# Performance work log

Hardware: AMD Instinct MI355X
Metric: run time of the kernel (lower is better)

## Reference

```python
import jax, jax.numpy as jnp
import numpy as np

C_IN, C_INT = 256, 128


def setup_inputs() -> dict:
    key = jax.random.key(0)
    ks = jax.random.split(key, 7)
    B, H, W = 8, 64, 64
    s_in = 1.0 / np.sqrt(C_IN)
    return {
        "x": jax.random.normal(ks[0], (B, C_IN, H, W), dtype=jnp.float32),
        "w_theta": jax.random.uniform(ks[1], (C_INT, C_IN), jnp.float32, -s_in, s_in),
        "b_theta": jax.random.uniform(ks[2], (C_INT,), jnp.float32, -s_in, s_in),
        "w_phi": jax.random.uniform(ks[3], (C_INT, C_IN), jnp.float32, -s_in, s_in),
        "b_phi": jax.random.uniform(ks[4], (C_INT,), jnp.float32, -s_in, s_in),
        "w_g": jax.random.uniform(ks[5], (C_INT, C_IN), jnp.float32, -s_in, s_in),
        "b_g": jax.random.uniform(ks[6], (C_INT,), jnp.float32, -s_in, s_in),
    }


def reference(x, w_theta, b_theta, w_phi, b_phi, w_g, b_g):
    B, C, H, W = x.shape
    # flatten spatial: [B, N, C], 1x1 conv == per-position linear
    xf = x.reshape(B, C, H * W).transpose(0, 2, 1)  # [B, N, C_in]
    theta = jnp.einsum('bnc,dc->bnd', xf, w_theta) + b_theta  # [B, N, C_int]
    phi = jnp.einsum('bnc,dc->bnd', xf, w_phi) + b_phi        # [B, N, C_int]
    g = jnp.einsum('bnc,dc->bnd', xf, w_g) + b_g              # [B, N, C_int]
    f = jnp.einsum('bnd,bmd->bnm', theta, phi)  # [B, N, N] unscaled scores
    f_div_C = jax.nn.softmax(f, axis=-1)
    y = jnp.einsum('bnm,bmd->bnd', f_div_C, g)  # [B, N, C_int]
    # back to [B, C_int, H, W]
    return y.transpose(0, 2, 1).reshape(B, C_INT, H, W)
```

## Files before the change

kernel.cpp:

```cpp
#include <hip/hip_runtime.h>

typedef __attribute__((ext_vector_type(8))) short bf8;
typedef __attribute__((ext_vector_type(4))) float f4;
typedef unsigned short u16;

constexpr int B_ = 8, CIN = 256, CINT = 128, NN = 4096;
constexpr float L2E = 1.44269504088896f;

__device__ __forceinline__ u16 f2bf(float f) {
  unsigned int u = __builtin_bit_cast(unsigned int, f);
  u += 0x7FFFu + ((u >> 16) & 1u);
  return (u16)(u >> 16);
}

__device__ __forceinline__ void glds16(const void* g, void* l) {
  __builtin_amdgcn_global_load_lds(
      (const __attribute__((address_space(1))) unsigned int*)g,
      (__attribute__((address_space(3))) unsigned int*)l, 16, 0, 0);
}

__device__ __forceinline__ int cvtpk(float lo, float hi) {
  int r;
  asm("v_cvt_pk_bf16_f32 %0, %1, %2" : "=v"(r) : "v"(lo), "v"(hi));
  return r;
}

__global__ __launch_bounds__(256) void prep_kernel(
    const float* __restrict__ wth, const float* __restrict__ wph,
    const float* __restrict__ wg, u16* __restrict__ wbf)
{
  int i = blockIdx.x * 256 + threadIdx.x;
  const float* src = (i < 32768) ? wth : (i < 65536) ? wph : wg;
  wbf[i] = f2bf(src[i & 32767]);
}

__global__ __launch_bounds__(256) void proj_kernel(
    const float* __restrict__ x, const u16* __restrict__ wbf,
    const float* __restrict__ bth, const float* __restrict__ bph,
    const float* __restrict__ bg,
    u16* __restrict__ theta, u16* __restrict__ phiT, u16* __restrict__ gTt)
{
  const int b = blockIdx.y, n0 = blockIdx.x * 64;
  const int tid = threadIdx.x, w = tid >> 6, l = tid & 63;
  const int lr = l & 15, lg = l >> 4;
  __shared__ __align__(16) u16 sx[64 * 256];

  const float* xb = x + (size_t)b * CIN * NN + n0;
  #pragma unroll
  for (int pass = 0; pass < 8; ++pass) {
    const int cb = w * 8 + pass * 32;
    u16 tmp[8];
    #pragma unroll
    for (int i = 0; i < 8; ++i) tmp[i] = f2bf(xb[(size_t)(cb + i) * NN + l]);
    uint4 v;
    v.x = (unsigned)tmp[0] | ((unsigned)tmp[1] << 16);
    v.y = (unsigned)tmp[2] | ((unsigned)tmp[3] << 16);
    v.z = (unsigned)tmp[4] | ((unsigned)tmp[5] << 16);
    v.w = (unsigned)tmp[6] | ((unsigned)tmp[7] << 16);
    *(uint4*)&sx[l * 256 + (((w + pass * 4) ^ (l & 7)) << 3)] = v;
  }
  __syncthreads();

  #pragma unroll
  for (int dti = 0; dti < 6; ++dti) {
    const int dt = w * 6 + dti;
    const int mat = dt >> 3, d0 = (dt & 7) * 16;
    const float* Bv = (mat == 0) ? bth : (mat == 1) ? bph : bg;
    const u16* wrow = wbf + mat * 32768 + (size_t)(d0 + lr) * 256 + lg * 8;
    bf8 wf[8];
    #pragma unroll
    for (int ks = 0; ks < 8; ++ks) wf[ks] = *(const bf8*)(wrow + ks * 32);

    #pragma unroll
    for (int mt = 0; mt < 4; ++mt) {
      f4 acc = {0.f, 0.f, 0.f, 0.f};
      const int row = mt * 16 + lr;
      #pragma unroll
      for (int ks = 0; ks < 8; ++ks) {
        bf8 bx = *(const bf8*)&sx[row * 256 + (((ks * 4 + lg) ^ (lr & 7)) << 3)];
        acc = __builtin_amdgcn_mfma_f32_16x16x32_bf16(wf[ks], bx, acc, 0, 0, 0);
      }
      const int m = n0 + mt * 16 + lr;
      const int dlo = d0 + lg * 4;
      if (mat == 0) {
        ushort4 h4;
        h4.x = f2bf(acc[0] + Bv[dlo + 0]);
        h4.y = f2bf(acc[1] + Bv[dlo + 1]);
        h4.z = f2bf(acc[2] + Bv[dlo + 2]);
        h4.w = f2bf(acc[3] + Bv[dlo + 3]);
        *(ushort4*)&theta[((size_t)b * NN + m) * CINT + dlo] = h4;
      } else if (mat == 1) {
        const int kt = m >> 5, r32 = m & 31;
        ushort4 h4;
        h4.x = f2bf((acc[0] + Bv[dlo + 0]) * L2E);
        h4.y = f2bf((acc[1] + Bv[dlo + 1]) * L2E);
        h4.z = f2bf((acc[2] + Bv[dlo + 2]) * L2E);
        h4.w = f2bf((acc[3] + Bv[dlo + 3]) * L2E);
        *(ushort4*)&phiT[((size_t)(b * 128 + kt)) * 4096 + r32 * 128 +
                         ((((dlo >> 3) ^ (r32 & 7))) << 3) + (dlo & 7)] = h4;
      } else {
        const int kt = m >> 5, kk = m & 31;
        #pragma unroll
        for (int r = 0; r < 4; ++r) {
          const int d = dlo + r;
          const int grow = d >> 1;
          const int chunk = (((d & 1) * 4 + (kk >> 3)) ^ (grow & 7));
          gTt[((size_t)(b * 128 + kt)) * 4096 + grow * 64 + chunk * 8 + (kk & 7)]
              = f2bf(acc[r] + Bv[d]);
        }
      }
    }
  }
}

__global__ __launch_bounds__(512, 2) void attn_kernel(
    const u16* __restrict__ theta, const u16* __restrict__ phiT,
    const u16* __restrict__ gTt, float* __restrict__ out)
{
  const int b  = blockIdx.y;
  const int t_ = threadIdx.x;
  const int w  = t_ >> 6;
  const int l  = t_ & 63;
  const int lr = l & 15, lg = l >> 4;
  const int h  = w >> 2, wq = w & 3;
  const int qw = blockIdx.x * 128 + wq * 32;

  __shared__ __align__(16) char smem[67584];
  u16* sphi_b = (u16*)smem;
  u16* sg_b   = (u16*)(smem + 32768);

  const u16* th = theta + (size_t)b * NN * CINT;
  bf8 qf[2][4];
  #pragma unroll
  for (int qt = 0; qt < 2; ++qt)
    #pragma unroll
    for (int ds = 0; ds < 4; ++ds)
      qf[qt][ds] = *(const bf8*)(th + (size_t)(qw + qt * 16 + lr) * CINT + ds * 32 + lg * 8);

  f4 y[2][8];
  #pragma unroll
  for (int qt = 0; qt < 2; ++qt)
    #pragma unroll
    for (int dt = 0; dt < 8; ++dt) y[qt][dt] = (f4){0.f, 0.f, 0.f, 0.f};
  float rs[2] = {0.f, 0.f};

  const char* psrc = (const char*)(phiT + (size_t)(b * 128 + h * 64) * 4096) +
                     wq * 2048 + l * 16;
  const char* gsrc = (const char*)(gTt + (size_t)(b * 128 + h * 64) * 4096) +
                     wq * 2048 + l * 16;

  #define STAGE(BUF, T)                                                    \
    {                                                                      \
      const char* sp = psrc + (size_t)(T) * 8192;                          \
      const char* sq = gsrc + (size_t)(T) * 8192;                          \
      char* lp = (char*)(sphi_b + (h * 2 + (BUF)) * 4096) + wq * 2048;     \
      char* lq = (char*)(sg_b + (h * 2 + (BUF)) * 4096) + wq * 2048;       \
      glds16(sp, lp); glds16(sp + 1024, lp + 1024);                        \
      glds16(sq, lq); glds16(sq + 1024, lq + 1024);                        \
    }

  STAGE(0, 0);
  asm volatile("s_waitcnt vmcnt(0)" ::: "memory");
  __builtin_amdgcn_s_barrier();
  __builtin_amdgcn_sched_barrier(0);

  int cur = 0;
  for (int t = 0; t < 64; ++t) {
    if (t < 63) STAGE(cur ^ 1, t + 1);

    const u16* PH = sphi_b + (h * 2 + cur) * 4096;
    const u16* GG = sg_b + (h * 2 + cur) * 4096;

    f4 s[2][2];
    s[0][0] = (f4){0.f,0.f,0.f,0.f}; s[0][1] = (f4){0.f,0.f,0.f,0.f};
    s[1][0] = (f4){0.f,0.f,0.f,0.f}; s[1][1] = (f4){0.f,0.f,0.f,0.f};
    __builtin_amdgcn_s_setprio(1);
    #pragma unroll
    for (int st = 0; st < 2; ++st) {
      const u16* base = PH + (st * 16 + lr) * 128;
      #pragma unroll
      for (int ds = 0; ds < 4; ++ds) {
        bf8 af = *(const bf8*)(base + (((ds * 4 + lg) ^ (lr & 7)) << 3));
        s[0][st] = __builtin_amdgcn_mfma_f32_16x16x32_bf16(af, qf[0][ds], s[0][st], 0, 0, 0);
        s[1][st] = __builtin_amdgcn_mfma_f32_16x16x32_bf16(af, qf[1][ds], s[1][st], 0, 0, 0);
      }
    }
    __builtin_amdgcn_s_setprio(0);

    bf8 gfr[8];
    #pragma unroll
    for (int dt = 0; dt < 8; ++dt) {
      const int grow = dt * 8 + (lr >> 1);
      const int chunk = (((lr & 1) * 4 + lg) ^ (grow & 7));
      gfr[dt] = *(const bf8*)(GG + grow * 64 + chunk * 8);
    }

    #pragma unroll
    for (int qt = 0; qt < 2; ++qt) {
      float p0 = __builtin_amdgcn_exp2f(s[qt][0][0]);
      float p1 = __builtin_amdgcn_exp2f(s[qt][0][1]);
      float p2 = __builtin_amdgcn_exp2f(s[qt][0][2]);
      float p3 = __builtin_amdgcn_exp2f(s[qt][0][3]);
      float p4 = __builtin_amdgcn_exp2f(s[qt][1][0]);
      float p5 = __builtin_amdgcn_exp2f(s[qt][1][1]);
      float p6 = __builtin_amdgcn_exp2f(s[qt][1][2]);
      float p7 = __builtin_amdgcn_exp2f(s[qt][1][3]);
      rs[qt] += ((p0 + p1) + (p2 + p3)) + ((p4 + p5) + (p6 + p7));

      int w0 = cvtpk(p0, p1), w1 = cvtpk(p2, p3);
      int w2 = cvtpk(p4, p5), w3 = cvtpk(p6, p7);
      asm volatile("v_permlane32_swap_b32 %0, %1" : "+v"(w0), "+v"(w2));
      asm volatile("v_permlane16_swap_b32 %0, %1" : "+v"(w0), "+v"(w2));
      asm volatile("v_permlane32_swap_b32 %0, %1" : "+v"(w1), "+v"(w3));
      asm volatile("v_permlane16_swap_b32 %0, %1" : "+v"(w1), "+v"(w3));
      int pai[4] = {w0, w1, w2, w3};
      bf8 paf = __builtin_bit_cast(bf8, *(int4*)pai);

      __builtin_amdgcn_s_setprio(1);
      #pragma unroll
      for (int dt = 0; dt < 8; ++dt)
        y[qt][dt] = __builtin_amdgcn_mfma_f32_16x16x32_bf16(paf, gfr[dt], y[qt][dt], 0, 0, 0);
      __builtin_amdgcn_s_setprio(0);
    }

    if (t < 63) asm volatile("s_waitcnt vmcnt(0)" ::: "memory");
    __builtin_amdgcn_s_barrier();
    __builtin_amdgcn_sched_barrier(0);
    cur ^= 1;
  }

  #pragma unroll
  for (int qt = 0; qt < 2; ++qt) {
    rs[qt] += __shfl_xor(rs[qt], 16);
    rs[qt] += __shfl_xor(rs[qt], 32);
  }
  __syncthreads();
  float* ycomb  = (float*)smem;
  float* rscomb = (float*)(smem + 65536);
  if (h == 1) {
    #pragma unroll
    for (int qt = 0; qt < 2; ++qt) {
      #pragma unroll
      for (int dt = 0; dt < 8; ++dt)
        *(f4*)&ycomb[wq * 4096 + (qt * 8 + dt) * 256 + l * 4] = y[qt][dt];
      rscomb[wq * 128 + qt * 64 + l] = rs[qt];
    }
  }
  __syncthreads();
  if (h == 0) {
    #pragma unroll
    for (int qt = 0; qt < 2; ++qt) {
      #pragma unroll
      for (int dt = 0; dt < 8; ++dt)
        y[qt][dt] += *(const f4*)&ycomb[wq * 4096 + (qt * 8 + dt) * 256 + l * 4];
      rs[qt] += rscomb[wq * 128 + qt * 64 + l];
    }
    float* ob = out + (size_t)b * CINT * NN;
    #pragma unroll
    for (int qt = 0; qt < 2; ++qt) {
      f4 rsi;
      #pragma unroll
      for (int r = 0; r < 4; ++r)
        rsi[r] = 1.0f / __shfl(rs[qt], lg * 4 + r, 64);
      #pragma unroll
      for (int dt = 0; dt < 8; ++dt) {
        f4 v = y[qt][dt] * rsi;
        *(float4*)&ob[(size_t)(dt * 16 + lr) * NN + qw + qt * 16 + lg * 4] = *(float4*)&v;
      }
    }
  }
}

extern "C" void kernel_launch(void* const* d_in, const int* in_sizes, int n_in,
                              void* d_out, int out_size, void* d_ws, size_t ws_size,
                              hipStream_t stream) {
  const float* x   = (const float*)d_in[0];
  const float* wth = (const float*)d_in[1];
  const float* bth = (const float*)d_in[2];
  const float* wph = (const float*)d_in[3];
  const float* bph = (const float*)d_in[4];
  const float* wg  = (const float*)d_in[5];
  const float* bg  = (const float*)d_in[6];
  float* out = (float*)d_out;

  u16* theta = (u16*)d_ws;
  u16* phiT  = theta + (size_t)B_ * NN * CINT;
  u16* gTt   = phiT  + (size_t)B_ * NN * CINT;
  u16* wbf   = gTt   + (size_t)B_ * NN * CINT;

  hipLaunchKernelGGL(prep_kernel, dim3(384), dim3(256), 0, stream, wth, wph, wg, wbf);
  hipLaunchKernelGGL(proj_kernel, dim3(64, 8), dim3(256), 0, stream,
                     x, wbf, bth, bph, bg, theta, phiT, gTt);
  hipLaunchKernelGGL(attn_kernel, dim3(32, 8), dim3(512), 0, stream,
                     theta, phiT, gTt, out);
}
```

Baseline: 104.7 us.

## Give each wave 64 queries over a quarter of keys to raise fragment reuse

Waves are repartitioned so each one processes four 16-query tiles over a quarter of the key range, instead of two tiles over half the keys. Each phi and g fragment read from LDS now feeds four MFMAs instead of two, which cuts LDS read traffic per unit of matrix work. Per-tile LDS staging doubles to about 132 KB, and the cross-wave reduction becomes a two-stage tree. The cost is much higher register pressure (128 fp32 accumulators plus 64 query registers) under the same launch bounds, and LDS use that likely allows only one block per CU, so spills or lost occupancy are possible.

```diff
diff --git a/kernel.cpp b/kernel.cpp
--- a/kernel.cpp
+++ b/kernel.cpp
@@ -122,41 +122,43 @@
   const int w  = t_ >> 6;
   const int l  = t_ & 63;
   const int lr = l & 15, lg = l >> 4;
-  const int h  = w >> 2, wq = w & 3;
-  const int qw = blockIdx.x * 128 + wq * 32;
-
-  __shared__ __align__(16) char smem[67584];
+  const int qs = w & 1, h = w >> 1;
+  const int q0 = blockIdx.x * 128 + qs * 64;
+
+  __shared__ __align__(16) char smem[135168];
   u16* sphi_b = (u16*)smem;
-  u16* sg_b   = (u16*)(smem + 32768);
+  u16* sg_b   = (u16*)(smem + 65536);
 
   const u16* th = theta + (size_t)b * NN * CINT;
-  bf8 qf[2][4];
-  #pragma unroll
-  for (int qt = 0; qt < 2; ++qt)
+  bf8 qf[4][4];
+  #pragma unroll
+  for (int qt = 0; qt < 4; ++qt)
     #pragma unroll
     for (int ds = 0; ds < 4; ++ds)
-      qf[qt][ds] = *(const bf8*)(th + (size_t)(qw + qt * 16 + lr) * CINT + ds * 32 + lg * 8);
-
-  f4 y[2][8];
-  #pragma unroll
-  for (int qt = 0; qt < 2; ++qt)
+      qf[qt][ds] = *(const bf8*)(th + (size_t)(q0 + qt * 16 + lr) * CINT + ds * 32 + lg * 8);
+
+  f4 y[4][8];
+  #pragma unroll
+  for (int qt = 0; qt < 4; ++qt)
     #pragma unroll
     for (int dt = 0; dt < 8; ++dt) y[qt][dt] = (f4){0.f, 0.f, 0.f, 0.f};
-  float rs[2] = {0.f, 0.f};
-
-  const char* psrc = (const char*)(phiT + (size_t)(b * 128 + h * 64) * 4096) +
-                     wq * 2048 + l * 16;
-  const char* gsrc = (const char*)(gTt + (size_t)(b * 128 + h * 64) * 4096) +
-                     wq * 2048 + l * 16;
+  float rs[4] = {0.f, 0.f, 0.f, 0.f};
+
+  const char* psrc = (const char*)(phiT + (size_t)(b * 128 + h * 32) * 4096) +
+                     qs * 4096 + l * 16;
+  const char* gsrc = (const char*)(gTt + (size_t)(b * 128 + h * 32) * 4096) +
+                     qs * 4096 + l * 16;
 
   #define STAGE(BUF, T)                                                    \
     {                                                                      \
       const char* sp = psrc + (size_t)(T) * 8192;                          \
       const char* sq = gsrc + (size_t)(T) * 8192;                          \
-      char* lp = (char*)(sphi_b + (h * 2 + (BUF)) * 4096) + wq * 2048;     \
-      char* lq = (char*)(sg_b + (h * 2 + (BUF)) * 4096) + wq * 2048;       \
-      glds16(sp, lp); glds16(sp + 1024, lp + 1024);                        \
-      glds16(sq, lq); glds16(sq + 1024, lq + 1024);                        \
+      char* lp = (char*)sphi_b + (h * 2 + (BUF)) * 8192 + qs * 4096;       \
+      char* lq = (char*)sg_b + (h * 2 + (BUF)) * 8192 + qs * 4096;         \
+      glds16(sp, lp);        glds16(sp + 1024, lp + 1024);                 \
+      glds16(sp + 2048, lp + 2048); glds16(sp + 3072, lp + 3072);          \
+      glds16(sq, lq);        glds16(sq + 1024, lq + 1024);                 \
+      glds16(sq + 2048, lq + 2048); glds16(sq + 3072, lq + 3072);          \
     }
 
   STAGE(0, 0);
@@ -165,99 +167,145 @@
   __builtin_amdgcn_sched_barrier(0);
 
   int cur = 0;
-  for (int t = 0; t < 64; ++t) {
-    if (t < 63) STAGE(cur ^ 1, t + 1);
+  for (int t = 0; t < 32; ++t) {
+    if (t < 31) STAGE(cur ^ 1, t + 1);
 
     const u16* PH = sphi_b + (h * 2 + cur) * 4096;
     const u16* GG = sg_b + (h * 2 + cur) * 4096;
 
-    f4 s[2][2];
-    s[0][0] = (f4){0.f,0.f,0.f,0.f}; s[0][1] = (f4){0.f,0.f,0.f,0.f};
-    s[1][0] = (f4){0.f,0.f,0.f,0.f}; s[1][1] = (f4){0.f,0.f,0.f,0.f};
-    __builtin_amdgcn_s_setprio(1);
-    #pragma unroll
-    for (int st = 0; st < 2; ++st) {
-      const u16* base = PH + (st * 16 + lr) * 128;
+    int pw0[4], pw1[4], pw2[4], pw3[4];
+
+    {
+      f4 s[4];
+      #pragma unroll
+      for (int qt = 0; qt < 4; ++qt) s[qt] = (f4){0.f, 0.f, 0.f, 0.f};
+      __builtin_amdgcn_s_setprio(1);
       #pragma unroll
       for (int ds = 0; ds < 4; ++ds) {
-        bf8 af = *(const bf8*)(base + (((ds * 4 + lg) ^ (lr & 7)) << 3));
-        s[0][st] = __builtin_amdgcn_mfma_f32_16x16x32_bf16(af, qf[0][ds], s[0][st], 0, 0, 0);
-        s[1][st] = __builtin_amdgcn_mfma_f32_16x16x32_bf16(af, qf[1][ds], s[1][st], 0, 0, 0);
-      }
-    }
-    __builtin_amdgcn_s_setprio(0);
-
-    bf8 gfr[8];
-    #pragma unroll
-    for (int dt = 0; dt < 8; ++dt) {
-      const int grow = dt * 8 + (lr >> 1);
-      const int chunk = (((lr & 1) * 4 + lg) ^ (grow & 7));
-      gfr[dt] = *(const bf8*)(GG + grow * 64 + chunk * 8);
-    }
-
-    #pragma unroll
-    for (int qt = 0; qt < 2; ++qt) {
-      float p0 = __builtin_amdgcn_exp2f(s[qt][0][0]);
-      float p1 = __builtin_amdgcn_exp2f(s[qt][0][1]);
-      float p2 = __builtin_amdgcn_exp2f(s[qt][0][2]);
-      float p3 = __builtin_amdgcn_exp2f(s[qt][0][3]);
-      float p4 = __builtin_amdgcn_exp2f(s[qt][1][0]);
-      float p5 = __builtin_amdgcn_exp2f(s[qt][1][1]);
-      float p6 = __builtin_amdgcn_exp2f(s[qt][1][2]);
-      float p7 = __builtin_amdgcn_exp2f(s[qt][1][3]);
-      rs[qt] += ((p0 + p1) + (p2 + p3)) + ((p4 + p5) + (p6 + p7));
-
-      int w0 = cvtpk(p0, p1), w1 = cvtpk(p2, p3);
-      int w2 = cvtpk(p4, p5), w3 = cvtpk(p6, p7);
+        bf8 af = *(const bf8*)(PH + lr * 128 + (((ds * 4 + lg) ^ (lr & 7)) << 3));
+        #pragma unroll
+        for (int qt = 0; qt < 4; ++qt)
+          s[qt] = __builtin_amdgcn_mfma_f32_16x16x32_bf16(af, qf[qt][ds], s[qt], 0, 0, 0);
+      }
+      __builtin_amdgcn_s_setprio(0);
+      #pragma unroll
+      for (int qt = 0; qt < 4; ++qt) {
+        float p0 = __builtin_amdgcn_exp2f(s[qt][0]);
+        float p1 = __builtin_amdgcn_exp2f(s[qt][1]);
+        float p2 = __builtin_amdgcn_exp2f(s[qt][2]);
+        float p3 = __builtin_amdgcn_exp2f(s[qt][3]);
+        rs[qt] += (p0 + p1) + (p2 + p3);
+        pw0[qt] = cvtpk(p0, p1);
+        pw1[qt] = cvtpk(p2, p3);
+      }
+    }
+    {
+      f4 s[4];
+      #pragma unroll
+      for (int qt = 0; qt < 4; ++qt) s[qt] = (f4){0.f, 0.f, 0.f, 0.f};
+      __builtin_amdgcn_s_setprio(1);
+      #pragma unroll
+      for (int ds = 0; ds < 4; ++ds) {
+        bf8 af = *(const bf8*)(PH + (16 + lr) * 128 + (((ds * 4 + lg) ^ (lr & 7)) << 3));
+        #pragma unroll
+        for (int qt = 0; qt < 4; ++qt)
+          s[qt] = __builtin_amdgcn_mfma_f32_16x16x32_bf16(af, qf[qt][ds], s[qt], 0, 0, 0);
+      }
+      __builtin_amdgcn_s_setprio(0);
+      #pragma unroll
+      for (int qt = 0; qt < 4; ++qt) {
+        float p0 = __builtin_amdgcn_exp2f(s[qt][0]);
+        float p1 = __builtin_amdgcn_exp2f(s[qt][1]);
+        float p2 = __builtin_amdgcn_exp2f(s[qt][2]);
+        float p3 = __builtin_amdgcn_exp2f(s[qt][3]);
+        rs[qt] += (p0 + p1) + (p2 + p3);
+        pw2[qt] = cvtpk(p0, p1);
+        pw3[qt] = cvtpk(p2, p3);
+      }
+    }
+
+    bf8 paf[4];
+    #pragma unroll
+    for (int qt = 0; qt < 4; ++qt) {
+      int w0 = pw0[qt], w1 = pw1[qt], w2 = pw2[qt], w3 = pw3[qt];
       asm volatile("v_permlane32_swap_b32 %0, %1" : "+v"(w0), "+v"(w2));
       asm volatile("v_permlane16_swap_b32 %0, %1" : "+v"(w0), "+v"(w2));
       asm volatile("v_permlane32_swap_b32 %0, %1" : "+v"(w1), "+v"(w3));
       asm volatile("v_permlane16_swap_b32 %0, %1" : "+v"(w1), "+v"(w3));
       int pai[4] = {w0, w1, w2, w3};
-      bf8 paf = __builtin_bit_cast(bf8, *(int4*)pai);
-
-      __builtin_amdgcn_s_setprio(1);
-      #pragma unroll
-      for (int dt = 0; dt < 8; ++dt)
-        y[qt][dt] = __builtin_amdgcn_mfma_f32_16x16x32_bf16(paf, gfr[dt], y[qt][dt], 0, 0, 0);
-      __builtin_amdgcn_s_setprio(0);
-    }
-
-    if (t < 63) asm volatile("s_waitcnt vmcnt(0)" ::: "memory");
+      paf[qt] = __builtin_bit_cast(bf8, *(int4*)pai);
+    }
+
+    __builtin_amdgcn_s_setprio(1);
+    #pragma unroll
+    for (int dt = 0; dt < 8; ++dt) {
+      const int grow = dt * 8 + (lr >> 1);
+      const int chunk = (((lr & 1) * 4 + lg) ^ (grow & 7));
+      bf8 gf = *(const bf8*)(GG + grow * 64 + (chunk << 3));
+      #pragma unroll
+      for (int qt = 0; qt < 4; ++qt)
+        y[qt][dt] = __builtin_amdgcn_mfma_f32_16x16x32_bf16(paf[qt], gf, y[qt][dt], 0, 0, 0);
+    }
+    __builtin_amdgcn_s_setprio(0);
+
+    asm volatile("s_waitcnt vmcnt(0)" ::: "memory");
     __builtin_amdgcn_s_barrier();
     __builtin_amdgcn_sched_barrier(0);
     cur ^= 1;
   }
 
   #pragma unroll
-  for (int qt = 0; qt < 2; ++qt) {
+  for (int qt = 0; qt < 4; ++qt) {
     rs[qt] += __shfl_xor(rs[qt], 16);
     rs[qt] += __shfl_xor(rs[qt], 32);
   }
   __syncthreads();
-  float* ycomb  = (float*)smem;
-  float* rscomb = (float*)(smem + 65536);
+  float* yc = (float*)smem;
+  float* rc = (float*)(smem + 131072);
+
+  if (h >= 2) {
+    const int slot = (h & 1) * 2 + qs;
+    #pragma unroll
+    for (int qt = 0; qt < 4; ++qt) {
+      #pragma unroll
+      for (int dt = 0; dt < 8; ++dt)
+        *(f4*)&yc[slot * 8192 + (qt * 8 + dt) * 256 + l * 4] = y[qt][dt];
+      rc[slot * 256 + qt * 64 + l] = rs[qt];
+    }
+  }
+  __syncthreads();
+  if (h < 2) {
+    const int slot = h * 2 + qs;
+    #pragma unroll
+    for (int qt = 0; qt < 4; ++qt) {
+      #pragma unroll
+      for (int dt = 0; dt < 8; ++dt)
+        y[qt][dt] += *(const f4*)&yc[slot * 8192 + (qt * 8 + dt) * 256 + l * 4];
+      rs[qt] += rc[slot * 256 + qt * 64 + l];
+    }
+  }
+  __syncthreads();
   if (h == 1) {
     #pragma unroll
-    for (int qt = 0; qt < 2; ++qt) {
+    for (int qt = 0; qt < 4; ++qt) {
       #pragma unroll
       for (int dt = 0; dt < 8; ++dt)
-        *(f4*)&ycomb[wq * 4096 + (qt * 8 + dt) * 256 + l * 4] = y[qt][dt];
-      rscomb[wq * 128 + qt * 64 + l] = rs[qt];
+        *(f4*)&yc[qs * 8192 + (qt * 8 + dt) * 256 + l * 4] = y[qt][dt];
+      rc[qs * 256 + qt * 64 + l] = rs[qt];
     }
   }
   __syncthreads();
   if (h == 0) {
     #pragma unroll
-    for (int qt = 0; qt < 2; ++qt) {
+    for (int qt = 0; qt < 4; ++qt) {
       #pragma unroll
       for (int dt = 0; dt < 8; ++dt)
-        y[qt][dt] += *(const f4*)&ycomb[wq * 4096 + (qt * 8 + dt) * 256 + l * 4];
-      rs[qt] += rscomb[wq * 128 + qt * 64 + l];
+        y[qt][dt] += *(const f4*)&yc[qs * 8192 + (qt * 8 + dt) * 256 + l * 4];
+      rs[qt] += rc[qs * 256 + qt * 64 + l];
     }
     float* ob = out + (size_t)b * CINT * NN;
     #pragma unroll
-    for (int qt = 0; qt < 2; ++qt) {
+    for (int qt = 0; qt < 4; ++qt) {
       f4 rsi;
       #pragma unroll
       for (int r = 0; r < 4; ++r)
@@ -265,7 +313,7 @@
       #pragma unroll
       for (int dt = 0; dt < 8; ++dt) {
         f4 v = y[qt][dt] * rsi;
-        *(float4*)&ob[(size_t)(dt * 16 + lr) * NN + qw + qt * 16 + lg * 4] = *(float4*)&v;
+        *(float4*)&ob[(size_t)(dt * 16 + lr) * NN + q0 + qt * 16 + lg * 4] = *(float4*)&v;
       }
     }
   }
```

After: 105.8 us. About the same (+1.1%).

## Split attention key range four ways in 1024-thread blocks

Applied to the files above, without the earlier changes.

The attention kernel now uses 1024-thread blocks. Each block splits the 4096 keys across four wave groups of 32 tiles each, instead of two groups of 64 tiles. Partial outputs and row sums are combined through LDS in a two-level reduction. The grid is flattened with batch interleaved into the block index. The goal is to double the waves resident per CU and halve the serial loop length, hiding latency better with the same 256-block grid. The cost is twice the LDS footprint (about 132 KB per block), which limits a CU to one block, plus an extra reduction stage and barriers.

```diff
diff --git a/kernel.cpp b/kernel.cpp
--- a/kernel.cpp
+++ b/kernel.cpp
@@ -113,21 +113,23 @@
   }
 }
 
-__global__ __launch_bounds__(512, 2) void attn_kernel(
+__global__ __launch_bounds__(1024, 4) void attn_kernel(
     const u16* __restrict__ theta, const u16* __restrict__ phiT,
     const u16* __restrict__ gTt, float* __restrict__ out)
 {
-  const int b  = blockIdx.y;
+  const int bid = blockIdx.x;
+  const int b   = bid & 7;
+  const int qtl = bid >> 3;
   const int t_ = threadIdx.x;
   const int w  = t_ >> 6;
   const int l  = t_ & 63;
   const int lr = l & 15, lg = l >> 4;
-  const int h  = w >> 2, wq = w & 3;
-  const int qw = blockIdx.x * 128 + wq * 32;
-
-  __shared__ __align__(16) char smem[67584];
+  const int qs = w & 3, h = w >> 2;
+  const int q0 = qtl * 128 + qs * 32;
+
+  __shared__ __align__(16) char smem[135168];
   u16* sphi_b = (u16*)smem;
-  u16* sg_b   = (u16*)(smem + 32768);
+  u16* sg_b   = (u16*)(smem + 65536);
 
   const u16* th = theta + (size_t)b * NN * CINT;
   bf8 qf[2][4];
@@ -135,7 +137,7 @@
   for (int qt = 0; qt < 2; ++qt)
     #pragma unroll
     for (int ds = 0; ds < 4; ++ds)
-      qf[qt][ds] = *(const bf8*)(th + (size_t)(qw + qt * 16 + lr) * CINT + ds * 32 + lg * 8);
+      qf[qt][ds] = *(const bf8*)(th + (size_t)(q0 + qt * 16 + lr) * CINT + ds * 32 + lg * 8);
 
   f4 y[2][8];
   #pragma unroll
@@ -144,17 +146,17 @@
     for (int dt = 0; dt < 8; ++dt) y[qt][dt] = (f4){0.f, 0.f, 0.f, 0.f};
   float rs[2] = {0.f, 0.f};
 
-  const char* psrc = (const char*)(phiT + (size_t)(b * 128 + h * 64) * 4096) +
-                     wq * 2048 + l * 16;
-  const char* gsrc = (const char*)(gTt + (size_t)(b * 128 + h * 64) * 4096) +
-                     wq * 2048 + l * 16;
+  const char* psrc = (const char*)(phiT + (size_t)(b * 128 + h * 32) * 4096) +
+                     qs * 2048 + l * 16;
+  const char* gsrc = (const char*)(gTt + (size_t)(b * 128 + h * 32) * 4096) +
+                     qs * 2048 + l * 16;
 
   #define STAGE(BUF, T)                                                    \
     {                                                                      \
       const char* sp = psrc + (size_t)(T) * 8192;                          \
       const char* sq = gsrc + (size_t)(T) * 8192;                          \
-      char* lp = (char*)(sphi_b + (h * 2 + (BUF)) * 4096) + wq * 2048;     \
-      char* lq = (char*)(sg_b + (h * 2 + (BUF)) * 4096) + wq * 2048;       \
+      char* lp = (char*)sphi_b + (h * 2 + (BUF)) * 8192 + qs * 2048;       \
+      char* lq = (char*)sg_b + (h * 2 + (BUF)) * 8192 + qs * 2048;         \
       glds16(sp, lp); glds16(sp + 1024, lp + 1024);                        \
       glds16(sq, lq); glds16(sq + 1024, lq + 1024);                        \
     }
@@ -165,8 +167,8 @@
   __builtin_amdgcn_sched_barrier(0);
 
   int cur = 0;
-  for (int t = 0; t < 64; ++t) {
-    if (t < 63) STAGE(cur ^ 1, t + 1);
+  for (int t = 0; t < 32; ++t) {
+    if (t < 31) STAGE(cur ^ 1, t + 1);
 
     const u16* PH = sphi_b + (h * 2 + cur) * 4096;
     const u16* GG = sg_b + (h * 2 + cur) * 4096;
@@ -192,7 +194,7 @@
     for (int dt = 0; dt < 8; ++dt) {
       const int grow = dt * 8 + (lr >> 1);
       const int chunk = (((lr & 1) * 4 + lg) ^ (grow & 7));
-      gfr[dt] = *(const bf8*)(GG + grow * 64 + chunk * 8);
+      gfr[dt] = *(const bf8*)(GG + grow * 64 + (chunk << 3));
     }
 
     #pragma unroll
@@ -223,7 +225,7 @@
       __builtin_amdgcn_s_setprio(0);
     }
 
-    if (t < 63) asm volatile("s_waitcnt vmcnt(0)" ::: "memory");
+    asm volatile("s_waitcnt vmcnt(0)" ::: "memory");
     __builtin_amdgcn_s_barrier();
     __builtin_amdgcn_sched_barrier(0);
     cur ^= 1;
@@ -235,15 +237,38 @@
     rs[qt] += __shfl_xor(rs[qt], 32);
   }
   __syncthreads();
-  float* ycomb  = (float*)smem;
-  float* rscomb = (float*)(smem + 65536);
+  float* yc = (float*)smem;
+  float* rc = (float*)(smem + 131072);
+
+  if (h >= 2) {
+    const int slot = (h - 2) * 4 + qs;
+    #pragma unroll
+    for (int qt = 0; qt < 2; ++qt) {
+      #pragma unroll
+      for (int dt = 0; dt < 8; ++dt)
+        *(f4*)&yc[slot * 4096 + (qt * 8 + dt) * 256 + l * 4] = y[qt][dt];
+      rc[slot * 128 + qt * 64 + l] = rs[qt];
+    }
+  }
+  __syncthreads();
+  if (h < 2) {
+    const int slot = h * 4 + qs;
+    #pragma unroll
+    for (int qt = 0; qt < 2; ++qt) {
+      #pragma unroll
+      for (int dt = 0; dt < 8; ++dt)
+        y[qt][dt] += *(const f4*)&yc[slot * 4096 + (qt * 8 + dt) * 256 + l * 4];
+      rs[qt] += rc[slot * 128 + qt * 64 + l];
+    }
+  }
+  __syncthreads();
   if (h == 1) {
     #pragma unroll
     for (int qt = 0; qt < 2; ++qt) {
       #pragma unroll
       for (int dt = 0; dt < 8; ++dt)
-        *(f4*)&ycomb[wq * 4096 + (qt * 8 + dt) * 256 + l * 4] = y[qt][dt];
-      rscomb[wq * 128 + qt * 64 + l] = rs[qt];
+        *(f4*)&yc[qs * 4096 + (qt * 8 + dt) * 256 + l * 4] = y[qt][dt];
+      rc[qs * 128 + qt * 64 + l] = rs[qt];
     }
   }
   __syncthreads();
@@ -252,8 +277,8 @@
     for (int qt = 0; qt < 2; ++qt) {
       #pragma unroll
       for (int dt = 0; dt < 8; ++dt)
-        y[qt][dt] += *(const f4*)&ycomb[wq * 4096 + (qt * 8 + dt) * 256 + l * 4];
-      rs[qt] += rscomb[wq * 128 + qt * 64 + l];
+        y[qt][dt] += *(const f4*)&yc[qs * 4096 + (qt * 8 + dt) * 256 + l * 4];
+      rs[qt] += rc[qs * 128 + qt * 64 + l];
     }
     float* ob = out + (size_t)b * CINT * NN;
     #pragma unroll
@@ -265,7 +290,7 @@
       #pragma unroll
       for (int dt = 0; dt < 8; ++dt) {
         f4 v = y[qt][dt] * rsi;
-        *(float4*)&ob[(size_t)(dt * 16 + lr) * NN + qw + qt * 16 + lg * 4] = *(float4*)&v;
+        *(float4*)&ob[(size_t)(dt * 16 + lr) * NN + q0 + qt * 16 + lg * 4] = *(float4*)&v;
       }
     }
   }
@@ -291,6 +316,6 @@
   hipLaunchKernelGGL(prep_kernel, dim3(384), dim3(256), 0, stream, wth, wph, wg, wbf);
   hipLaunchKernelGGL(proj_kernel, dim3(64, 8), dim3(256), 0, stream,
                      x, wbf, bth, bph, bg, theta, phiT, gTt);
-  hipLaunchKernelGGL(attn_kernel, dim3(32, 8), dim3(512), 0, stream,
+  hipLaunchKernelGGL(attn_kernel, dim3(256), dim3(1024), 0, stream,
                      theta, phiT, gTt, out);
 }
```

Measured after the change: 247.9 us. 2.37x slower.

## Double key tile to 64 in attention loop with new phi/g layouts

Applied to the files above, without the earlier changes.

The attention kernel now processes 64 keys per iteration instead of 32. This halves the number of loop iterations and barriers, and the g values are read straight from LDS in a transposed, swizzled layout. The projection kernel writes phiT and gTt in matching 64-row tiles. The grid is flattened so batch index is the fastest-varying part of the block id, and LDS grows to 128KB per block. This likely drops occupancy from two blocks per CU to one, in exchange for fewer synchronisations and more MFMA work per barrier.

```diff
diff --git a/kernel.cpp b/kernel.cpp
--- a/kernel.cpp
+++ b/kernel.cpp
@@ -90,23 +90,21 @@
         h4.w = f2bf(acc[3] + Bv[dlo + 3]);
         *(ushort4*)&theta[((size_t)b * NN + m) * CINT + dlo] = h4;
       } else if (mat == 1) {
-        const int kt = m >> 5, r32 = m & 31;
+        const int kt = m >> 6, rr = m & 63;
         ushort4 h4;
         h4.x = f2bf((acc[0] + Bv[dlo + 0]) * L2E);
         h4.y = f2bf((acc[1] + Bv[dlo + 1]) * L2E);
         h4.z = f2bf((acc[2] + Bv[dlo + 2]) * L2E);
         h4.w = f2bf((acc[3] + Bv[dlo + 3]) * L2E);
-        *(ushort4*)&phiT[((size_t)(b * 128 + kt)) * 4096 + r32 * 128 +
-                         ((((dlo >> 3) ^ (r32 & 7))) << 3) + (dlo & 7)] = h4;
+        *(ushort4*)&phiT[((size_t)(b * 64 + kt)) * 8192 + rr * 128 +
+                         ((((dlo >> 3) ^ (rr & 7))) << 3) + (dlo & 7)] = h4;
       } else {
-        const int kt = m >> 5, kk = m & 31;
+        const int kt = m >> 6, rr = m & 63;
         #pragma unroll
         for (int r = 0; r < 4; ++r) {
           const int d = dlo + r;
-          const int grow = d >> 1;
-          const int chunk = (((d & 1) * 4 + (kk >> 3)) ^ (grow & 7));
-          gTt[((size_t)(b * 128 + kt)) * 4096 + grow * 64 + chunk * 8 + (kk & 7)]
-              = f2bf(acc[r] + Bv[d]);
+          gTt[((size_t)(b * 64 + kt)) * 8192 + d * 64 +
+              (((rr >> 3) ^ (d & 7)) << 3) + (rr & 7)] = f2bf(acc[r] + Bv[d]);
         }
       }
     }
@@ -117,17 +115,19 @@
     const u16* __restrict__ theta, const u16* __restrict__ phiT,
     const u16* __restrict__ gTt, float* __restrict__ out)
 {
-  const int b  = blockIdx.y;
+  const int bid = blockIdx.x;
+  const int b   = bid & 7;
+  const int qtl = bid >> 3;
   const int t_ = threadIdx.x;
   const int w  = t_ >> 6;
   const int l  = t_ & 63;
   const int lr = l & 15, lg = l >> 4;
   const int h  = w >> 2, wq = w & 3;
-  const int qw = blockIdx.x * 128 + wq * 32;
-
-  __shared__ __align__(16) char smem[67584];
+  const int qw = qtl * 128 + wq * 32;
+
+  __shared__ __align__(16) char smem[131072];
   u16* sphi_b = (u16*)smem;
-  u16* sg_b   = (u16*)(smem + 32768);
+  u16* sg_b   = (u16*)(smem + 65536);
 
   const u16* th = theta + (size_t)b * NN * CINT;
   bf8 qf[2][4];
@@ -144,19 +144,21 @@
     for (int dt = 0; dt < 8; ++dt) y[qt][dt] = (f4){0.f, 0.f, 0.f, 0.f};
   float rs[2] = {0.f, 0.f};
 
-  const char* psrc = (const char*)(phiT + (size_t)(b * 128 + h * 64) * 4096) +
-                     wq * 2048 + l * 16;
-  const char* gsrc = (const char*)(gTt + (size_t)(b * 128 + h * 64) * 4096) +
-                     wq * 2048 + l * 16;
-
-  #define STAGE(BUF, T)                                                    \
-    {                                                                      \
-      const char* sp = psrc + (size_t)(T) * 8192;                          \
-      const char* sq = gsrc + (size_t)(T) * 8192;                          \
-      char* lp = (char*)(sphi_b + (h * 2 + (BUF)) * 4096) + wq * 2048;     \
-      char* lq = (char*)(sg_b + (h * 2 + (BUF)) * 4096) + wq * 2048;       \
-      glds16(sp, lp); glds16(sp + 1024, lp + 1024);                        \
-      glds16(sq, lq); glds16(sq + 1024, lq + 1024);                        \
+  const char* psrc = (const char*)(phiT + (size_t)(b * 64 + h * 32) * 8192) +
+                     wq * 4096 + l * 16;
+  const char* gsrc = (const char*)(gTt + (size_t)(b * 64 + h * 32) * 8192) +
+                     wq * 4096 + l * 16;
+
+  #define STAGE(BUF, T)                                                     \
+    {                                                                       \
+      const char* sp = psrc + (size_t)(T) * 16384;                          \
+      const char* sq = gsrc + (size_t)(T) * 16384;                          \
+      char* lp = (char*)sphi_b + (h * 2 + (BUF)) * 16384 + wq * 4096;       \
+      char* lq = (char*)sg_b + (h * 2 + (BUF)) * 16384 + wq * 4096;         \
+      glds16(sp, lp);        glds16(sp + 1024, lp + 1024);                  \
+      glds16(sp + 2048, lp + 2048); glds16(sp + 3072, lp + 3072);           \
+      glds16(sq, lq);        glds16(sq + 1024, lq + 1024);                  \
+      glds16(sq + 2048, lq + 2048); glds16(sq + 3072, lq + 3072);           \
     }
 
   STAGE(0, 0);
@@ -165,18 +167,20 @@
   __builtin_amdgcn_sched_barrier(0);
 
   int cur = 0;
-  for (int t = 0; t < 64; ++t) {
-    if (t < 63) STAGE(cur ^ 1, t + 1);
-
-    const u16* PH = sphi_b + (h * 2 + cur) * 4096;
-    const u16* GG = sg_b + (h * 2 + cur) * 4096;
-
-    f4 s[2][2];
-    s[0][0] = (f4){0.f,0.f,0.f,0.f}; s[0][1] = (f4){0.f,0.f,0.f,0.f};
-    s[1][0] = (f4){0.f,0.f,0.f,0.f}; s[1][1] = (f4){0.f,0.f,0.f,0.f};
+  for (int t = 0; t < 32; ++t) {
+    if (t < 31) STAGE(cur ^ 1, t + 1);
+
+    const u16* PH = sphi_b + (h * 2 + cur) * 8192;
+    const u16* GG = sg_b + (h * 2 + cur) * 8192;
+
+    f4 s[2][4];
+    #pragma unroll
+    for (int qt = 0; qt < 2; ++qt)
+      #pragma unroll
+      for (int st = 0; st < 4; ++st) s[qt][st] = (f4){0.f, 0.f, 0.f, 0.f};
     __builtin_amdgcn_s_setprio(1);
     #pragma unroll
-    for (int st = 0; st < 2; ++st) {
+    for (int st = 0; st < 4; ++st) {
       const u16* base = PH + (st * 16 + lr) * 128;
       #pragma unroll
       for (int ds = 0; ds < 4; ++ds) {
@@ -187,43 +191,46 @@
     }
     __builtin_amdgcn_s_setprio(0);
 
-    bf8 gfr[8];
-    #pragma unroll
-    for (int dt = 0; dt < 8; ++dt) {
-      const int grow = dt * 8 + (lr >> 1);
-      const int chunk = (((lr & 1) * 4 + lg) ^ (grow & 7));
-      gfr[dt] = *(const bf8*)(GG + grow * 64 + chunk * 8);
-    }
-
+    bf8 paf[2][2];
     #pragma unroll
     for (int qt = 0; qt < 2; ++qt) {
-      float p0 = __builtin_amdgcn_exp2f(s[qt][0][0]);
-      float p1 = __builtin_amdgcn_exp2f(s[qt][0][1]);
-      float p2 = __builtin_amdgcn_exp2f(s[qt][0][2]);
-      float p3 = __builtin_amdgcn_exp2f(s[qt][0][3]);
-      float p4 = __builtin_amdgcn_exp2f(s[qt][1][0]);
-      float p5 = __builtin_amdgcn_exp2f(s[qt][1][1]);
-      float p6 = __builtin_amdgcn_exp2f(s[qt][1][2]);
-      float p7 = __builtin_amdgcn_exp2f(s[qt][1][3]);
-      rs[qt] += ((p0 + p1) + (p2 + p3)) + ((p4 + p5) + (p6 + p7));
-
-      int w0 = cvtpk(p0, p1), w1 = cvtpk(p2, p3);
-      int w2 = cvtpk(p4, p5), w3 = cvtpk(p6, p7);
-      asm volatile("v_permlane32_swap_b32 %0, %1" : "+v"(w0), "+v"(w2));
-      asm volatile("v_permlane16_swap_b32 %0, %1" : "+v"(w0), "+v"(w2));
-      asm volatile("v_permlane32_swap_b32 %0, %1" : "+v"(w1), "+v"(w3));
-      asm volatile("v_permlane16_swap_b32 %0, %1" : "+v"(w1), "+v"(w3));
-      int pai[4] = {w0, w1, w2, w3};
-      bf8 paf = __builtin_bit_cast(bf8, *(int4*)pai);
-
-      __builtin_amdgcn_s_setprio(1);
-      #pragma unroll
-      for (int dt = 0; dt < 8; ++dt)
-        y[qt][dt] = __builtin_amdgcn_mfma_f32_16x16x32_bf16(paf, gfr[dt], y[qt][dt], 0, 0, 0);
-      __builtin_amdgcn_s_setprio(0);
-    }
-
-    if (t < 63) asm volatile("s_waitcnt vmcnt(0)" ::: "memory");
+      #pragma unroll
+      for (int pr = 0; pr < 2; ++pr) {
+        float p0 = __builtin_amdgcn_exp2f(s[qt][2 * pr][0]);
+        float p1 = __builtin_amdgcn_exp2f(s[qt][2 * pr][1]);
+        float p2 = __builtin_amdgcn_exp2f(s[qt][2 * pr][2]);
+        float p3 = __builtin_amdgcn_exp2f(s[qt][2 * pr][3]);
+        float p4 = __builtin_amdgcn_exp2f(s[qt][2 * pr + 1][0]);
+        float p5 = __builtin_amdgcn_exp2f(s[qt][2 * pr + 1][1]);
+        float p6 = __builtin_amdgcn_exp2f(s[qt][2 * pr + 1][2]);
+        float p7 = __builtin_amdgcn_exp2f(s[qt][2 * pr + 1][3]);
+        rs[qt] += ((p0 + p1) + (p2 + p3)) + ((p4 + p5) + (p6 + p7));
+
+        int w0 = cvtpk(p0, p1), w1 = cvtpk(p2, p3);
+        int w2 = cvtpk(p4, p5), w3 = cvtpk(p6, p7);
+        asm volatile("v_permlane32_swap_b32 %0, %1" : "+v"(w0), "+v"(w2));
+        asm volatile("v_permlane16_swap_b32 %0, %1" : "+v"(w0), "+v"(w2));
+        asm volatile("v_permlane32_swap_b32 %0, %1" : "+v"(w1), "+v"(w3));
+        asm volatile("v_permlane16_swap_b32 %0, %1" : "+v"(w1), "+v"(w3));
+        int pai[4] = {w0, w1, w2, w3};
+        paf[qt][pr] = __builtin_bit_cast(bf8, *(int4*)pai);
+      }
+    }
+
+    __builtin_amdgcn_s_setprio(1);
+    #pragma unroll
+    for (int ks = 0; ks < 2; ++ks) {
+      #pragma unroll
+      for (int dt = 0; dt < 8; ++dt) {
+        bf8 gf = *(const bf8*)(GG + (dt * 16 + lr) * 64 +
+                               (((ks * 4 + lg) ^ (lr & 7)) << 3));
+        y[0][dt] = __builtin_amdgcn_mfma_f32_16x16x32_bf16(paf[0][ks], gf, y[0][dt], 0, 0, 0);
+        y[1][dt] = __builtin_amdgcn_mfma_f32_16x16x32_bf16(paf[1][ks], gf, y[1][dt], 0, 0, 0);
+      }
+    }
+    __builtin_amdgcn_s_setprio(0);
+
+    asm volatile("s_waitcnt vmcnt(0)" ::: "memory");
     __builtin_amdgcn_s_barrier();
     __builtin_amdgcn_sched_barrier(0);
     cur ^= 1;
@@ -235,15 +242,15 @@
     rs[qt] += __shfl_xor(rs[qt], 32);
   }
   __syncthreads();
-  float* ycomb  = (float*)smem;
-  float* rscomb = (float*)(smem + 65536);
+  float* yc = (float*)smem;
+  float* rc = (float*)(smem + 65536);
   if (h == 1) {
     #pragma unroll
     for (int qt = 0; qt < 2; ++qt) {
       #pragma unroll
       for (int dt = 0; dt < 8; ++dt)
-        *(f4*)&ycomb[wq * 4096 + (qt * 8 + dt) * 256 + l * 4] = y[qt][dt];
-      rscomb[wq * 128 + qt * 64 + l] = rs[qt];
+        *(f4*)&yc[wq * 4096 + (qt * 8 + dt) * 256 + l * 4] = y[qt][dt];
+      rc[wq * 128 + qt * 64 + l] = rs[qt];
     }
   }
   __syncthreads();
@@ -252,8 +259,8 @@
     for (int qt = 0; qt < 2; ++qt) {
       #pragma unroll
       for (int dt = 0; dt < 8; ++dt)
-        y[qt][dt] += *(const f4*)&ycomb[wq * 4096 + (qt * 8 + dt) * 256 + l * 4];
-      rs[qt] += rscomb[wq * 128 + qt * 64 + l];
+        y[qt][dt] += *(const f4*)&yc[wq * 4096 + (qt * 8 + dt) * 256 + l * 4];
+      rs[qt] += rc[wq * 128 + qt * 64 + l];
     }
     float* ob = out + (size_t)b * CINT * NN;
     #pragma unroll
@@ -291,6 +298,6 @@
   hipLaunchKernelGGL(prep_kernel, dim3(384), dim3(256), 0, stream, wth, wph, wg, wbf);
   hipLaunchKernelGGL(proj_kernel, dim3(64, 8), dim3(256), 0, stream,
                      x, wbf, bth, bph, bg, theta, phiT, gTt);
-  hipLaunchKernelGGL(attn_kernel, dim3(32, 8), dim3(512), 0, stream,
+  hipLaunchKernelGGL(attn_kernel, dim3(256), dim3(512), 0, stream,
                      theta, phiT, gTt, out);
 }
```

Result: no change. 105.3 us (+0.6%).
